# Kernel tuning notes

Hardware: AMD Instinct MI355X
Metric: run time of the kernel (lower is better)

## Reference

```python
import jax, jax.numpy as jnp
import numpy as np
from functools import lru_cache
from jax.scipy.linalg import expm

N_QUBITS = 6
DIM = 2 ** N_QUBITS          # 64
N_PAULI = 4 ** N_QUBITS      # 4096


@lru_cache(maxsize=None)
def _pauli_tensor_np(n_qubits):
    # All n-qubit Pauli strings as dense matrices, ordered base-4
    # (digit 0..3 -> I, X, Y, Z; most-significant digit = first qubit).
    I = np.eye(2, dtype=np.complex64)
    X = np.array([[0, 1], [1, 0]], dtype=np.complex64)
    Y = np.array([[0, -1j], [1j, 0]], dtype=np.complex64)
    Z = np.array([[1, 0], [0, -1]], dtype=np.complex64)
    base = np.stack([I, X, Y, Z])  # [4,2,2]
    T = base
    for _ in range(n_qubits - 1):
        k, d = T.shape[0], T.shape[1]
        T = np.einsum('iab,jcd->ijacbd', T, base).reshape(k * 4, d * 2, d * 2)
    return np.ascontiguousarray(T.astype(np.complex64))  # [4^n, 2^n, 2^n]


def setup_inputs() -> dict:
    key = jax.random.key(0)
    kx, kw, kb = jax.random.split(key, 3)
    x = jax.random.normal(kx, (512, 4000), dtype=jnp.float32)
    weight = jax.random.normal(kw, (4, N_PAULI - 1), dtype=jnp.float32)
    bias = jax.random.normal(kb, (DIM,), dtype=jnp.float32)
    return {"x": x, "weight": weight, "bias": bias}


def reference(x, weight, bias):
    # x: [B, in_dim] float32; weight: [n_reps, 4^n - 1]; bias: [out_dim]
    B, in_dim = x.shape
    n_reps = weight.shape[0]
    out_dim = bias.shape[0]
    P = jnp.asarray(_pauli_tensor_np(N_QUBITS))  # [4096, 64, 64] complex64

    # Pad data coefficients up to the full Pauli basis (identity included).
    xp = jnp.pad(x, ((0, 0), (0, N_PAULI - in_dim))).astype(jnp.complex64)

    # Data-encoding Hamiltonian per sample: H_d[b] = sum_p x[b,p] * P[p]
    Hd = jnp.einsum('bp,pij->bij', xp, P)                       # [B,64,64]
    Ud = jax.vmap(expm)(-1j * Hd)                               # [B,64,64]

    # Trainable Hamiltonians per rep (identity Pauli excluded -> global phase).
    Hp = jnp.einsum('rp,pij->rij', weight.astype(jnp.complex64), P[1:])
    Up = jax.vmap(expm)(-1j * Hp)                               # [R,64,64]

    # Data re-uploading circuit on |0...0>: repeat (U_param @ U_data).
    psi = jnp.zeros((B, DIM), dtype=jnp.complex64).at[:, 0].set(1.0)
    for r in range(n_reps):
        psi = jnp.einsum('bij,bj->bi', Ud, psi)
        psi = jnp.einsum('ij,bj->bi', Up[r], psi)

    # Observables are computational-basis projectors |k><k|, k < out_dim:
    # <psi|O_k|psi> = |psi_k|^2
    probs = (psi[:, :out_dim].real ** 2 + psi[:, :out_dim].imag ** 2)
    return probs.astype(jnp.float32) + bias
```

## Files before the change

kernel.cpp:

```cpp
#include <hip/hip_runtime.h>
#include <math.h>

typedef float2 cplx;
typedef __attribute__((ext_vector_type(8))) short short8v;
typedef __attribute__((ext_vector_type(4))) short short4v;
typedef __attribute__((ext_vector_type(4))) float float4v;

#define IN_DIM 4000
#define NREPS 4

#define C0f  1.0f
#define C1f  1.0f
#define C2f  0.5f
#define C3f  0.16666667f
#define C4f  0.041666668f
#define C5f  8.3333333e-3f
#define C6f  1.3888889e-3f
#define C7f  1.9841270e-4f
#define C8f  2.4801587e-5f
#define C9f  2.7557319e-6f
#define C10f 2.7557319e-7f
#define C11f 2.5052108e-8f
#define C12f 2.0876757e-9f
#define C13f 1.6059044e-10f
#define C14f 1.1470746e-11f
#define C15f 7.6471637e-13f

#define MFMA(A,B,C) __builtin_amdgcn_mfma_f32_16x16x32_bf16((A),(B),(C),0,0,0)


__device__ __forceinline__ int idxSw(int a, int b) {
    return (a << 6) + ((((b >> 3) + a) & 7) << 3) + (b & 7);
}
__device__ __forceinline__ short f2bf(float f) {
    unsigned u = __float_as_uint(f);
    return (short)((u + 0x7FFF + ((u >> 16) & 1)) >> 16);
}
__device__ __forceinline__ float bf2f(short s) {
    return __uint_as_float(((unsigned)(unsigned short)s) << 16);
}
__device__ __forceinline__ short8v neg8(short8v a) {
    int4 u; __builtin_memcpy(&u, &a, 16);
    u.x ^= 0x80008000; u.y ^= 0x80008000; u.z ^= 0x80008000; u.w ^= 0x80008000;
    short8v r; __builtin_memcpy(&r, &u, 16); return r;
}

template<int AM, int BM, int NDM, int NDN>
__device__ __forceinline__ void mm_mfma(const short* __restrict__ As,
                                        const short* __restrict__ Bs,
                                        int li, int q, int mb, int nb,
                                        float4v* __restrict__ accR,
                                        float4v* __restrict__ accI)
{
    #pragma unroll
    for (int ks = 0; ks < 2; ks++) {
        const int ch = ks * 4 + q;
        short8v arh[NDM], arl[NDM], cRh[NDM], cRl[NDM], cIh[NDM], cIl[NDM];
        #pragma unroll
        for (int dm = 0; dm < NDM; dm++) {
            int r = ((mb + dm) << 4) + li;
            int off = (r << 6) + (((ch + r) & 7) << 3);
            arh[dm] = *(const short8v*)(As + off);
            arl[dm] = *(const short8v*)(As + 4096 + off);
            short8v aih = *(const short8v*)(As + 8192 + off);
            short8v ail = *(const short8v*)(As + 12288 + off);
            short8v nih = neg8(aih), nil_ = neg8(ail);
            cRh[dm] = (AM == 2) ? aih : nih;
            cRl[dm] = (AM == 2) ? ail : nil_;
            cIh[dm] = (AM == 2) ? nih : aih;
            cIl[dm] = (AM == 2) ? nil_ : ail;
        }
        #pragma unroll
        for (int dn = 0; dn < NDN; dn++) {
            int n = ((nb + dn) << 4) + li;
            int off = (n << 6) + (((ch + n) & 7) << 3);
            short8v brh = *(const short8v*)(Bs + off);
            short8v brl = *(const short8v*)(Bs + 4096 + off);
            short8v bih = *(const short8v*)(Bs + 8192 + off);
            short8v bil = *(const short8v*)(Bs + 12288 + off);
            if (BM == 1) { brh = neg8(brh); brl = neg8(brl); }
            __builtin_amdgcn_s_setprio(1);
            #pragma unroll
            for (int dm = 0; dm < NDM; dm++) {
                int ti = dm * NDN + dn;
                accR[ti] = MFMA(arh[dm], brh, accR[ti]);
                accR[ti] = MFMA(arh[dm], brl, accR[ti]);
                accR[ti] = MFMA(arl[dm], brh, accR[ti]);
                accR[ti] = MFMA(cRh[dm], bih, accR[ti]);
                accR[ti] = MFMA(cRh[dm], bil, accR[ti]);
                accR[ti] = MFMA(cRl[dm], bih, accR[ti]);
                accI[ti] = MFMA(arh[dm], bih, accI[ti]);
                accI[ti] = MFMA(arh[dm], bil, accI[ti]);
                accI[ti] = MFMA(arl[dm], bih, accI[ti]);
                accI[ti] = MFMA(cIh[dm], brh, accI[ti]);
                accI[ti] = MFMA(cIh[dm], brl, accI[ti]);
                accI[ti] = MFMA(cIl[dm], brh, accI[ti]);
            }
            __builtin_amdgcn_s_setprio(0);
        }
    }
}

template<int NDM, int NDN>
__device__ __forceinline__ void write_row(short* __restrict__ S, int li, int q,
                                          int mb, int nb,
                                          const float4v* cre, const float4v* cim)
{
    #pragma unroll
    for (int dm = 0; dm < NDM; dm++)
    #pragma unroll
    for (int dn = 0; dn < NDN; dn++) {
        int ti = dm * NDN + dn;
        int c = ((nb + dn) << 4) + li;
        #pragma unroll
        for (int reg = 0; reg < 4; reg++) {
            int r = ((mb + dm) << 4) + q * 4 + reg;
            int off = idxSw(r, c);
            float vr = cre[ti][reg], vi = cim[ti][reg];
            short rh = f2bf(vr), rl = f2bf(vr - bf2f(rh));
            short ih = f2bf(vi), il = f2bf(vi - bf2f(ih));
            S[off] = rh; S[4096 + off] = rl; S[8192 + off] = ih; S[12288 + off] = il;
        }
    }
}

template<int NDM, int NDN>
__device__ __forceinline__ void write_rowT(short* __restrict__ S, int li, int q,
                                           int mb, int nb,
                                           const float4v* cre, const float4v* cim)
{
    #pragma unroll
    for (int dm = 0; dm < NDM; dm++)
    #pragma unroll
    for (int dn = 0; dn < NDN; dn++) {
        int ti = dm * NDN + dn;
        int c = ((nb + dn) << 4) + li;
        int k0 = ((mb + dm) << 4) + q * 4;
        int off = idxSw(c, k0);
        short4v rh, rl, ih, il;
        #pragma unroll
        for (int reg = 0; reg < 4; reg++) {
            float vr = cre[ti][reg], vi = cim[ti][reg];
            short h1 = f2bf(vr); rh[reg] = h1; rl[reg] = f2bf(vr - bf2f(h1));
            short h2 = f2bf(vi); ih[reg] = h2; il[reg] = f2bf(vi - bf2f(h2));
        }
        *(short4v*)(S + off) = rh;
        *(short4v*)(S + 4096 + off) = rl;
        *(short4v*)(S + 8192 + off) = ih;
        *(short4v*)(S + 12288 + off) = il;
    }
}

template<int NDM, int NDN>
__device__ __forceinline__ void gather_tile(const short* __restrict__ S, int li, int q,
                                            int mb, int nb, float4v* bre, float4v* bim)
{
    #pragma unroll
    for (int dm = 0; dm < NDM; dm++)
    #pragma unroll
    for (int dn = 0; dn < NDN; dn++) {
        int ti = dm * NDN + dn;
        int c = ((nb + dn) << 4) + li;
        #pragma unroll
        for (int reg = 0; reg < 4; reg++) {
            int r = ((mb + dm) << 4) + q * 4 + reg;
            int off = idxSw(r, c);
            bre[ti][reg] = bf2f(S[off]) + bf2f(S[4096 + off]);
            bim[ti][reg] = bf2f(S[8192 + off]) + bf2f(S[12288 + off]);
        }
    }
}

template<int NDM, int NDN>
__device__ __forceinline__ void adddiag(float4v* u, float cI, int li, int q, int mb, int nb)
{
    #pragma unroll
    for (int dm = 0; dm < NDM; dm++)
    #pragma unroll
    for (int dn = 0; dn < NDN; dn++) {
        if (mb + dm == nb + dn) {
            #pragma unroll
            for (int e = 0; e < 4; e++)
                if (li == q * 4 + e) u[dm * NDN + dn][e] += cI;
        }
    }
}

template<int NDM, int NDN>
__device__ __forceinline__ void store_tiles(cplx* __restrict__ dst, int li, int q,
                                            int mb, int nb,
                                            const float4v* ure, const float4v* uim)
{
    #pragma unroll
    for (int dm = 0; dm < NDM; dm++)
    #pragma unroll
    for (int dn = 0; dn < NDN; dn++) {
        int ti = dm * NDN + dn;
        int c = ((nb + dn) << 4) + li;
        int cs = c ^ (((c >> 4) & 1) << 1);
        #pragma unroll
        for (int reg = 0; reg < 4; reg++) {
            int r = ((mb + dm) << 4) + q * 4 + reg;
            dst[(r << 6) + cs] = make_float2(ure[ti][reg], uim[ti][reg]);
        }
    }
}

__device__ __forceinline__ cplx pauli_phase(float v, int xm, int zm) {
    int ny = __popc(xm & zm) & 3;
    if (ny == 0) return make_float2(v, 0.f);
    if (ny == 1) return make_float2(0.f, -v);
    if (ny == 2) return make_float2(-v, 0.f);
    return make_float2(0.f, v);
}

__device__ __forceinline__ void expm_core8(char* __restrict__ LDS,
                                           const float* __restrict__ src, bool isW,
                                           int t, float4v* ure, float4v* uim)
{
    constexpr int NDM = 1, NDN = 2, NT = 2;
    short* S0 = (short*)LDS;
    short* S1 = (short*)(LDS + 32768);
    cplx*  W  = (cplx*)(LDS + 32768);
    float* red = (float*)(LDS + 65536);
    const int lane = t & 63, wv = t >> 6;
    const int li = lane & 15, q = lane >> 4;
    const int mb = wv & 3, nb = (wv >> 2) << 1;

    float sumsq = 0.f;
    #pragma unroll
    for (int n = 0; n < 8; n++) {
        int p = t + 512 * n;
        int xm = 0, zm = 0;
        #pragma unroll
        for (int k = 0; k < 6; k++) {
            int d = (p >> (2 * k)) & 3;
            int hi = d >> 1, lo = d & 1;
            zm |= hi << k; xm |= (hi ^ lo) << k;
        }
        float v = isW ? ((p == 0) ? 0.f : src[p - 1])
                      : ((p < IN_DIM) ? src[p] : 0.f);
        sumsq += v * v;
        W[(xm << 6) + zm] = pauli_phase(v, xm, zm);
    }
    #pragma unroll
    for (int d = 32; d >= 1; d >>= 1) sumsq += __shfl_xor(sumsq, d, 64);
    if (lane == 0) red[wv] = sumsq;
    __syncthreads();

    float rs = 0.f;
    #pragma unroll
    for (int i2 = 0; i2 < 8; i2++) rs += red[i2];
    float fro = sqrtf(64.f * rs);
    int s1 = 0; { float nn = fro; while (nn > 8.f && s1 < 24) { nn *= 0.5f; s1++; } }
    float sc1 = exp2f((float)(-s1));

    cplx hv[8];
    #pragma unroll
    for (int rr = 0; rr < 8; rr++) hv[rr] = W[((wv * 8 + rr) << 6) + lane];
    #pragma unroll
    for (int d = 1; d < 64; d <<= 1) {
        float sg = (lane & d) ? -1.f : 1.f;
        #pragma unroll
        for (int rr = 0; rr < 8; rr++) {
            float px = __shfl_xor(hv[rr].x, d, 64);
            float py = __shfl_xor(hv[rr].y, d, 64);
            hv[rr].x = fmaf(sg, hv[rr].x, px);
            hv[rr].y = fmaf(sg, hv[rr].y, py);
        }
    }

    #pragma unroll
    for (int rr = 0; rr < 8; rr++) {
        int m = wv * 8 + rr;
        int c = lane ^ m;
        float vr = hv[rr].y * sc1, vi = -hv[rr].x * sc1;
        short rh = f2bf(vr), rl = f2bf(vr - bf2f(rh));
        short ih = f2bf(vi), il = f2bf(vi - bf2f(ih));
        int off = idxSw(lane, c);
        S0[off] = rh; S0[4096 + off] = rl; S0[8192 + off] = ih; S0[12288 + off] = il;
    }
    __syncthreads();

    const float4v z4 = {0.f, 0.f, 0.f, 0.f};
    float4v accR[NT], accI[NT];
    #define ZERO_ACC _Pragma("unroll") for (int i2 = 0; i2 < NT; i2++) { accR[i2]=z4; accI[i2]=z4; }

    ZERO_ACC
    mm_mfma<0, 1, NDM, NDN>(S0, S0, li, q, mb, nb, accR, accI);
    float ss = 0.f;
    #pragma unroll
    for (int ti = 0; ti < NT; ti++)
        #pragma unroll
        for (int e = 0; e < 4; e++)
            ss += accR[ti][e]*accR[ti][e] + accI[ti][e]*accI[ti][e];
    #pragma unroll
    for (int d = 32; d >= 1; d >>= 1) ss += __shfl_xor(ss, d, 64);
    if (lane == 0) red[8 + wv] = ss;
    __syncthreads();

    rs = 0.f;
    #pragma unroll
    for (int i2 = 0; i2 < 8; i2++) rs += red[8 + i2];
    float bound = sqrtf(sqrtf(rs));
    int ds = 0; { float nn = bound; while (nn > 3.4f && ds < 12) { nn *= 0.5f; ds++; } }
    const int s = s1 + ds;
    float dsc = exp2f((float)(-ds)), dsc2 = dsc * dsc;

    float4v bre[NT], bim[NT];
    gather_tile<NDM, NDN>(S0, li, q, mb, nb, bre, bim);

    #pragma unroll
    for (int ti = 0; ti < NT; ti++) { ure[ti] = accR[ti] * dsc2; uim[ti] = accI[ti] * dsc2; }
    write_rowT<NDM, NDN>(S1, li, q, mb, nb, ure, uim);
    __syncthreads();

    {
        float ca = C15f * dsc;
        #pragma unroll
        for (int ti = 0; ti < NT; ti++) { ure[ti] = ca * bre[ti]; uim[ti] = ca * bim[ti]; }
        adddiag<NDM, NDN>(ure, C14f, li, q, mb, nb);
        write_rowT<NDM, NDN>(S0, li, q, mb, nb, ure, uim);
    }
    __syncthreads();

    const float cIc[7] = { C0f, C2f, C4f, C6f, C8f, C10f, C12f };
    const float cAc[7] = { C1f, C3f, C5f, C7f, C9f, C11f, C13f };
    for (int j = 6; j >= 0; j--) {
        ZERO_ACC
        mm_mfma<2, 0, NDM, NDN>(S1, S0, li, q, mb, nb, accR, accI);
        __syncthreads();
        float ca = cAc[j] * dsc, cI = cIc[j];
        #pragma unroll
        for (int ti = 0; ti < NT; ti++) {
            ure[ti] = accR[ti] + ca * bre[ti];
            uim[ti] = accI[ti] + ca * bim[ti];
        }
        adddiag<NDM, NDN>(ure, cI, li, q, mb, nb);
        write_rowT<NDM, NDN>(S0, li, q, mb, nb, ure, uim);
        __syncthreads();
    }

    for (int sq = 0; sq < s; sq++) {
        write_row<NDM, NDN>(S1, li, q, mb, nb, ure, uim);
        if (sq > 0) write_rowT<NDM, NDN>(S0, li, q, mb, nb, ure, uim);
        __syncthreads();
        ZERO_ACC
        mm_mfma<0, 0, NDM, NDN>(S1, S0, li, q, mb, nb, accR, accI);
        __syncthreads();
        #pragma unroll
        for (int ti = 0; ti < NT; ti++) { ure[ti] = accR[ti]; uim[ti] = accI[ti]; }
    }
    #undef ZERO_ACC
}

__device__ __forceinline__ cplx matvec_wave8(const cplx* __restrict__ M,
                                             const cplx* __restrict__ pin,
                                             int lane, int wv)
{
    const int ri = lane & 7;
    const int rr = (wv << 3) + ri;
    const int kc = lane >> 3;
    const int ch = (kc + ri) & 7;
    const int b  = (ch >> 1) & 1;
    const float4* Mr = (const float4*)(M + (rr << 6)) + (ch << 2);
    float4 m0 = Mr[0 ^ b], m1 = Mr[1 ^ b], m2 = Mr[2 ^ b], m3 = Mr[3 ^ b];
    const cplx* p = pin + (ch << 3);
    cplx p0 = p[0], p1 = p[1], p2 = p[2], p3 = p[3];
    cplx p4 = p[4], p5 = p[5], p6 = p[6], p7 = p[7];
    float ax = 0.f, ay = 0.f;
    ax = fmaf(m0.x, p0.x, fmaf(-m0.y, p0.y, ax));
    ay = fmaf(m0.x, p0.y, fmaf( m0.y, p0.x, ay));
    ax = fmaf(m0.z, p1.x, fmaf(-m0.w, p1.y, ax));
    ay = fmaf(m0.z, p1.y, fmaf( m0.w, p1.x, ay));
    ax = fmaf(m1.x, p2.x, fmaf(-m1.y, p2.y, ax));
    ay = fmaf(m1.x, p2.y, fmaf( m1.y, p2.x, ay));
    ax = fmaf(m1.z, p3.x, fmaf(-m1.w, p3.y, ax));
    ay = fmaf(m1.z, p3.y, fmaf( m1.w, p3.x, ay));
    ax = fmaf(m2.x, p4.x, fmaf(-m2.y, p4.y, ax));
    ay = fmaf(m2.x, p4.y, fmaf( m2.y, p4.x, ay));
    ax = fmaf(m2.z, p5.x, fmaf(-m2.w, p5.y, ax));
    ay = fmaf(m2.z, p5.y, fmaf( m2.w, p5.x, ay));
    ax = fmaf(m3.x, p6.x, fmaf(-m3.y, p6.y, ax));
    ay = fmaf(m3.x, p6.y, fmaf( m3.y, p6.x, ay));
    ax = fmaf(m3.z, p7.x, fmaf(-m3.w, p7.y, ax));
    ay = fmaf(m3.z, p7.y, fmaf( m3.w, p7.x, ay));
    ax += __shfl_xor(ax, 8, 64);  ay += __shfl_xor(ay, 8, 64);
    ax += __shfl_xor(ax, 16, 64); ay += __shfl_xor(ay, 16, 64);
    ax += __shfl_xor(ax, 32, 64); ay += __shfl_xor(ay, 32, 64);
    return make_float2(ax, ay);
}

__global__ __launch_bounds__(512, 4) void circuit_kernel(const float* __restrict__ x,
                                                         const float* __restrict__ w,
                                                         const float* __restrict__ bias,
                                                         cplx* __restrict__ ws,
                                                         int* __restrict__ flag,
                                                         float* __restrict__ out)
{
    __shared__ float4 LDSf4[4168];
    char* LDS = (char*)LDSf4;
    const int t = threadIdx.x, b = blockIdx.x;
    const int lane = t & 63, wv = t >> 6, li = lane & 15, q = lane >> 4;
    const int mb = wv & 3, nb = (wv >> 2) << 1;
    float4v ure[2], uim[2];

    for (int duty = (b < NREPS) ? 0 : 1; duty < 2; duty++) {
        const bool isW = (duty == 0);
        const float* src = isW ? (w + (size_t)b * 4095) : (x + (size_t)b * IN_DIM);
        expm_core8(LDS, src, isW, t, ure, uim);
        if (isW) {
            store_tiles<1, 2>(ws + ((size_t)b << 12), li, q, mb, nb, ure, uim);
            __syncthreads();
            if (t == 0)
                __hip_atomic_fetch_add(flag, 1, __ATOMIC_RELEASE, __HIP_MEMORY_SCOPE_AGENT);
        }
    }

    cplx* Ud   = (cplx*)(LDS + 32768);
    cplx* UpS  = (cplx*)LDS;
    cplx* psiA = (cplx*)(LDS + 65664);
    cplx* psiB = (cplx*)(LDS + 66176);

    store_tiles<1, 2>(Ud, li, q, mb, nb, ure, uim);
    if (t < 64) psiA[t] = make_float2(t == 0 ? 1.f : 0.f, 0.f);
    if (t == 0) {
        while (__hip_atomic_load(flag, __ATOMIC_ACQUIRE, __HIP_MEMORY_SCOPE_AGENT) < NREPS)
            __builtin_amdgcn_s_sleep(8);
    }
    __syncthreads();

    const int rowi = (wv << 3) + (lane & 7);
    for (int r = 0; r < NREPS; r++) {
        {
            const float4* srcv = (const float4*)(ws + ((size_t)r << 12));
            float4* dstY = (float4*)UpS;
            #pragma unroll
            for (int n = 0; n < 4; n++) dstY[n * 512 + t] = srcv[n * 512 + t];
        }
        cplx v1 = matvec_wave8(Ud, psiA, lane, wv);
        if (lane < 8) psiB[rowi] = v1;
        __syncthreads();
        cplx v2 = matvec_wave8(UpS, psiB, lane, wv);
        if (lane < 8) psiA[rowi] = v2;
        __syncthreads();
    }
    if (t < 64) {
        cplx pv = psiA[t];
        out[(b << 6) + t] = fmaf(pv.x, pv.x, fmaf(pv.y, pv.y, bias[t]));
    }
}

extern "C" void kernel_launch(void* const* d_in, const int* in_sizes, int n_in,
                              void* d_out, int out_size, void* d_ws, size_t ws_size,
                              hipStream_t stream)
{
    const float* x    = (const float*)d_in[0];
    const float* w    = (const float*)d_in[1];
    const float* bias = (const float*)d_in[2];
    float* out = (float*)d_out;
    cplx* ws   = (cplx*)d_ws;
    int* flag  = (int*)((char*)d_ws + (NREPS << 15));

    int B = in_sizes[0] / IN_DIM;

    hipMemsetAsync(flag, 0, sizeof(int), stream);
    hipLaunchKernelGGL(circuit_kernel, dim3(B), dim3(512), 0, stream,
                       x, w, bias, ws, flag, out);
}
```

Measured before the change: 153.8 us.

## Split parameter-unitary expm into separate 1024-thread kernel, drop in-kernel flag spin

Moves the four trainable-Hamiltonian matrix exponentials out of the fused circuit kernel into a separate up_kernel with 1024 threads (16 waves, one 16x16 tile each) and 128KB LDS. The main kernel no longer has blocks 0-3 doing double work or blocks spinning on an atomic flag, and the memset is removed. The cost is an extra kernel launch and a serialization point between the kernels: the data expm can no longer overlap with the parameter expm.

```diff
diff --git a/kernel.cpp b/kernel.cpp
--- a/kernel.cpp
+++ b/kernel.cpp
@@ -44,6 +44,15 @@
     u.x ^= 0x80008000; u.y ^= 0x80008000; u.z ^= 0x80008000; u.w ^= 0x80008000;
     short8v r; __builtin_memcpy(&r, &u, 16); return r;
 }
+
+__device__ __forceinline__ cplx pauli_phase(float v, int xm, int zm) {
+    int ny = __popc(xm & zm) & 3;
+    if (ny == 0) return make_float2(v, 0.f);
+    if (ny == 1) return make_float2(0.f, -v);
+    if (ny == 2) return make_float2(-v, 0.f);
+    return make_float2(0.f, v);
+}
+
 
 template<int AM, int BM, int NDM, int NDN>
 __device__ __forceinline__ void mm_mfma(const short* __restrict__ As,
@@ -206,14 +215,6 @@
     }
 }
 
-__device__ __forceinline__ cplx pauli_phase(float v, int xm, int zm) {
-    int ny = __popc(xm & zm) & 3;
-    if (ny == 0) return make_float2(v, 0.f);
-    if (ny == 1) return make_float2(0.f, -v);
-    if (ny == 2) return make_float2(-v, 0.f);
-    return make_float2(0.f, v);
-}
-
 __device__ __forceinline__ void expm_core8(char* __restrict__ LDS,
                                            const float* __restrict__ src, bool isW,
                                            int t, float4v* ure, float4v* uim)
@@ -269,7 +270,6 @@
             hv[rr].y = fmaf(sg, hv[rr].y, py);
         }
     }
-
     #pragma unroll
     for (int rr = 0; rr < 8; rr++) {
         int m = wv * 8 + rr;
@@ -350,6 +350,257 @@
         __syncthreads();
         #pragma unroll
         for (int ti = 0; ti < NT; ti++) { ure[ti] = accR[ti]; uim[ti] = accI[ti]; }
+    }
+    #undef ZERO_ACC
+}
+
+
+template<int AM, int BM>
+__device__ __forceinline__ void mm_mfma1(const short* __restrict__ As,
+                                         const short* __restrict__ Bs,
+                                         int li, int q, int mb, int nb,
+                                         float4v* __restrict__ accR,
+                                         float4v* __restrict__ accI)
+{
+    #pragma unroll
+    for (int ks = 0; ks < 2; ks++) {
+        const int ch = ks * 4 + q;
+        int r = (mb << 4) + li;
+        int offA = (r << 6) + (((ch + r) & 7) << 3);
+        short8v arh = *(const short8v*)(As + offA);
+        short8v arl = *(const short8v*)(As + 4096 + offA);
+        short8v aih = *(const short8v*)(As + 8192 + offA);
+        short8v ail = *(const short8v*)(As + 12288 + offA);
+        short8v nih = neg8(aih), nil_ = neg8(ail);
+        short8v cRh = (AM == 2) ? aih : nih;
+        short8v cRl = (AM == 2) ? ail : nil_;
+        short8v cIh = (AM == 2) ? nih : aih;
+        short8v cIl = (AM == 2) ? nil_ : ail;
+
+        int n = (nb << 4) + li;
+        int offB = (n << 6) + (((ch + n) & 7) << 3);
+        short8v brh = *(const short8v*)(Bs + offB);
+        short8v brl = *(const short8v*)(Bs + 4096 + offB);
+        short8v bih = *(const short8v*)(Bs + 8192 + offB);
+        short8v bil = *(const short8v*)(Bs + 12288 + offB);
+        if (BM == 1) { brh = neg8(brh); brl = neg8(brl); }
+
+        accR[0] = MFMA(arh, brh, accR[0]);
+        accR[0] = MFMA(arh, brl, accR[0]);
+        accR[0] = MFMA(arl, brh, accR[0]);
+        accR[0] = MFMA(cRh, bih, accR[0]);
+        accR[0] = MFMA(cRh, bil, accR[0]);
+        accR[0] = MFMA(cRl, bih, accR[0]);
+        accI[0] = MFMA(arh, bih, accI[0]);
+        accI[0] = MFMA(arh, bil, accI[0]);
+        accI[0] = MFMA(arl, bih, accI[0]);
+        accI[0] = MFMA(cIh, brh, accI[0]);
+        accI[0] = MFMA(cIh, brl, accI[0]);
+        accI[0] = MFMA(cIl, brh, accI[0]);
+    }
+}
+
+__device__ __forceinline__ void write_row1(short* __restrict__ S, int li, int q,
+                                           int mb, int nb,
+                                           const float4v* cre, const float4v* cim)
+{
+    int c = (nb << 4) + li;
+    #pragma unroll
+    for (int reg = 0; reg < 4; reg++) {
+        int r = (mb << 4) + q * 4 + reg;
+        int off = idxSw(r, c);
+        float vr = cre[0][reg], vi = cim[0][reg];
+        short rh = f2bf(vr), rl = f2bf(vr - bf2f(rh));
+        short ih = f2bf(vi), il = f2bf(vi - bf2f(ih));
+        S[off] = rh; S[4096 + off] = rl; S[8192 + off] = ih; S[12288 + off] = il;
+    }
+}
+
+__device__ __forceinline__ void write_rowT1(short* __restrict__ S, int li, int q,
+                                            int mb, int nb,
+                                            const float4v* cre, const float4v* cim)
+{
+    int c = (nb << 4) + li;
+    int k0 = (mb << 4) + q * 4;
+    int off = idxSw(c, k0);
+    short4v rh, rl, ih, il;
+    #pragma unroll
+    for (int reg = 0; reg < 4; reg++) {
+        float vr = cre[0][reg], vi = cim[0][reg];
+        short h1 = f2bf(vr); rh[reg] = h1; rl[reg] = f2bf(vr - bf2f(h1));
+        short h2 = f2bf(vi); ih[reg] = h2; il[reg] = f2bf(vi - bf2f(h2));
+    }
+    *(short4v*)(S + off) = rh;
+    *(short4v*)(S + 4096 + off) = rl;
+    *(short4v*)(S + 8192 + off) = ih;
+    *(short4v*)(S + 12288 + off) = il;
+}
+
+__device__ __forceinline__ void gather_tile1(const short* __restrict__ S, int li, int q,
+                                             int mb, int nb, float4v* bre, float4v* bim)
+{
+    int c = (nb << 4) + li;
+    #pragma unroll
+    for (int reg = 0; reg < 4; reg++) {
+        int r = (mb << 4) + q * 4 + reg;
+        int off = idxSw(r, c);
+        bre[0][reg] = bf2f(S[off]) + bf2f(S[4096 + off]);
+        bim[0][reg] = bf2f(S[8192 + off]) + bf2f(S[12288 + off]);
+    }
+}
+
+__device__ __forceinline__ void adddiag1(float4v* u, float cI, int li, int q, int mb, int nb)
+{
+    if (mb == nb) {
+        #pragma unroll
+        for (int e = 0; e < 4; e++)
+            if (li == q * 4 + e) u[0][e] += cI;
+    }
+}
+
+__device__ __forceinline__ void store_tiles1(cplx* __restrict__ dst, int li, int q,
+                                             int mb, int nb,
+                                             const float4v* ure, const float4v* uim)
+{
+    int c = (nb << 4) + li;
+    int cs = c ^ (((c >> 4) & 1) << 1);
+    #pragma unroll
+    for (int reg = 0; reg < 4; reg++) {
+        int r = (mb << 4) + q * 4 + reg;
+        dst[(r << 6) + cs] = make_float2(ure[0][reg], uim[0][reg]);
+    }
+}
+
+__device__ __forceinline__ void expm_core16(char* __restrict__ LDS,
+                                            const float* __restrict__ src, bool isW,
+                                            int t, float4v* ure, float4v* uim)
+{
+    short* P0 = (short*)LDS;
+    short* P1 = (short*)(LDS + 32768);
+    short* P2 = (short*)(LDS + 65536);
+    short* P3 = (short*)(LDS + 98304);
+    cplx*  W  = (cplx*)(LDS + 65536);
+    float* red = (float*)(LDS + 98304);
+    const int lane = t & 63, wv = t >> 6;
+    const int li = lane & 15, q = lane >> 4;
+    const int mb = wv & 3, nb = wv >> 2;
+
+    float sumsq = 0.f;
+    #pragma unroll
+    for (int n = 0; n < 4; n++) {
+        int p = t + 1024 * n;
+        int xm = 0, zm = 0;
+        #pragma unroll
+        for (int k = 0; k < 6; k++) {
+            int d = (p >> (2 * k)) & 3;
+            int hi = d >> 1, lo = d & 1;
+            zm |= hi << k; xm |= (hi ^ lo) << k;
+        }
+        float v = isW ? ((p == 0) ? 0.f : src[p - 1])
+                      : ((p < IN_DIM) ? src[p] : 0.f);
+        sumsq += v * v;
+        W[(xm << 6) + zm] = pauli_phase(v, xm, zm);
+    }
+    #pragma unroll
+    for (int d = 32; d >= 1; d >>= 1) sumsq += __shfl_xor(sumsq, d, 64);
+    if (lane == 0) red[wv] = sumsq;
+    __syncthreads();
+
+    float rs = 0.f;
+    #pragma unroll
+    for (int i2 = 0; i2 < 16; i2++) rs += red[i2];
+    float fro = sqrtf(64.f * rs);
+    int s1 = 0; { float nn = fro; while (nn > 8.f && s1 < 24) { nn *= 0.5f; s1++; } }
+    float sc1 = exp2f((float)(-s1));
+
+    cplx hv[4];
+    #pragma unroll
+    for (int rr = 0; rr < 4; rr++) hv[rr] = W[((wv * 4 + rr) << 6) + lane];
+    #pragma unroll
+    for (int d = 1; d < 64; d <<= 1) {
+        float sg = (lane & d) ? -1.f : 1.f;
+        #pragma unroll
+        for (int rr = 0; rr < 4; rr++) {
+            float px = __shfl_xor(hv[rr].x, d, 64);
+            float py = __shfl_xor(hv[rr].y, d, 64);
+            hv[rr].x = fmaf(sg, hv[rr].x, px);
+            hv[rr].y = fmaf(sg, hv[rr].y, py);
+        }
+    }
+    #pragma unroll
+    for (int rr = 0; rr < 4; rr++) {
+        int m = wv * 4 + rr;
+        int c = lane ^ m;
+        float vr = hv[rr].y * sc1, vi = -hv[rr].x * sc1;
+        short rh = f2bf(vr), rl = f2bf(vr - bf2f(rh));
+        short ih = f2bf(vi), il = f2bf(vi - bf2f(ih));
+        int off = idxSw(lane, c);
+        P0[off] = rh; P0[4096 + off] = rl; P0[8192 + off] = ih; P0[12288 + off] = il;
+    }
+    __syncthreads();
+
+    const float4v z4 = {0.f, 0.f, 0.f, 0.f};
+    float4v accR[1], accI[1];
+    #define ZERO_ACC { accR[0] = z4; accI[0] = z4; }
+
+    ZERO_ACC
+    mm_mfma1<0, 1>(P0, P0, li, q, mb, nb, accR, accI);
+    write_rowT1(P1, li, q, mb, nb, accR, accI);
+    float ss = 0.f;
+    #pragma unroll
+    for (int e = 0; e < 4; e++)
+        ss += accR[0][e]*accR[0][e] + accI[0][e]*accI[0][e];
+    #pragma unroll
+    for (int d = 32; d >= 1; d >>= 1) ss += __shfl_xor(ss, d, 64);
+    if (lane == 0) red[16 + wv] = ss;
+    __syncthreads();
+
+    rs = 0.f;
+    #pragma unroll
+    for (int i2 = 0; i2 < 16; i2++) rs += red[16 + i2];
+    float bound = sqrtf(sqrtf(rs));
+    int ds = 0; { float nn = bound; while (nn > 3.4f && ds < 12) { nn *= 0.5f; ds++; } }
+    const int s = s1 + ds;
+    float dsc = exp2f((float)(-ds)), dsc2 = dsc * dsc;
+
+    float4v bre[1], bim[1];
+    gather_tile1(P0, li, q, mb, nb, bre, bim);
+
+    {
+        float ca = C15f * dsc;
+        ure[0] = ca * bre[0]; uim[0] = ca * bim[0];
+        adddiag1(ure, C14f, li, q, mb, nb);
+        write_rowT1(P2, li, q, mb, nb, ure, uim);
+    }
+    __syncthreads();
+
+    const float cIc[7] = { C0f, C2f, C4f, C6f, C8f, C10f, C12f };
+    const float cAc[7] = { C1f, C3f, C5f, C7f, C9f, C11f, C13f };
+    short* Vr = P2; short* Vw = P3;
+    for (int j = 6; j >= 0; j--) {
+        ZERO_ACC
+        mm_mfma1<2, 0>(P1, Vr, li, q, mb, nb, accR, accI);
+        float ca = cAc[j] * dsc, cI = cIc[j];
+        ure[0] = dsc2 * accR[0] + ca * bre[0];
+        uim[0] = dsc2 * accI[0] + ca * bim[0];
+        adddiag1(ure, cI, li, q, mb, nb);
+        if (j > 0) {
+            write_rowT1(Vw, li, q, mb, nb, ure, uim);
+            short* tmp = Vr; Vr = Vw; Vw = tmp;
+        }
+        __syncthreads();
+    }
+
+    for (int sq = 0; sq < s; sq++) {
+        short* Ua = (sq & 1) ? P2 : P0;
+        short* Ub = (sq & 1) ? P3 : P1;
+        write_row1(Ua, li, q, mb, nb, ure, uim);
+        write_rowT1(Ub, li, q, mb, nb, ure, uim);
+        __syncthreads();
+        ZERO_ACC
+        mm_mfma1<0, 0>(Ua, Ub, li, q, mb, nb, accR, accI);
+        __syncthreads();
+        ure[0] = accR[0]; uim[0] = accI[0];
     }
     #undef ZERO_ACC
 }
@@ -391,11 +642,22 @@
     return make_float2(ax, ay);
 }
 
+__global__ __launch_bounds__(1024) void up_kernel(const float* __restrict__ w,
+                                                  cplx* __restrict__ ws)
+{
+    __shared__ float4 LDSf4[8192];
+    char* LDS = (char*)LDSf4;
+    const int t = threadIdx.x, r = blockIdx.x;
+    const int lane = t & 63, wv = t >> 6, li = lane & 15, q = lane >> 4;
+    const int mb = wv & 3, nb = wv >> 2;
+    float4v ure[1], uim[1];
+    expm_core16(LDS, w + (size_t)r * 4095, true, t, ure, uim);
+    store_tiles1(ws + ((size_t)r << 12), li, q, mb, nb, ure, uim);
+}
+
 __global__ __launch_bounds__(512, 4) void circuit_kernel(const float* __restrict__ x,
-                                                         const float* __restrict__ w,
+                                                         const cplx* __restrict__ ws,
                                                          const float* __restrict__ bias,
-                                                         cplx* __restrict__ ws,
-                                                         int* __restrict__ flag,
                                                          float* __restrict__ out)
 {
     __shared__ float4 LDSf4[4168];
@@ -405,17 +667,7 @@
     const int mb = wv & 3, nb = (wv >> 2) << 1;
     float4v ure[2], uim[2];
 
-    for (int duty = (b < NREPS) ? 0 : 1; duty < 2; duty++) {
-        const bool isW = (duty == 0);
-        const float* src = isW ? (w + (size_t)b * 4095) : (x + (size_t)b * IN_DIM);
-        expm_core8(LDS, src, isW, t, ure, uim);
-        if (isW) {
-            store_tiles<1, 2>(ws + ((size_t)b << 12), li, q, mb, nb, ure, uim);
-            __syncthreads();
-            if (t == 0)
-                __hip_atomic_fetch_add(flag, 1, __ATOMIC_RELEASE, __HIP_MEMORY_SCOPE_AGENT);
-        }
-    }
+    expm_core8(LDS, x + (size_t)b * IN_DIM, false, t, ure, uim);
 
     cplx* Ud   = (cplx*)(LDS + 32768);
     cplx* UpS  = (cplx*)LDS;
@@ -424,10 +676,6 @@
 
     store_tiles<1, 2>(Ud, li, q, mb, nb, ure, uim);
     if (t < 64) psiA[t] = make_float2(t == 0 ? 1.f : 0.f, 0.f);
-    if (t == 0) {
-        while (__hip_atomic_load(flag, __ATOMIC_ACQUIRE, __HIP_MEMORY_SCOPE_AGENT) < NREPS)
-            __builtin_amdgcn_s_sleep(8);
-    }
     __syncthreads();
 
     const int rowi = (wv << 3) + (lane & 7);
@@ -460,11 +708,9 @@
     const float* bias = (const float*)d_in[2];
     float* out = (float*)d_out;
     cplx* ws   = (cplx*)d_ws;
-    int* flag  = (int*)((char*)d_ws + (NREPS << 15));
 
     int B = in_sizes[0] / IN_DIM;
 
-    hipMemsetAsync(flag, 0, sizeof(int), stream);
-    hipLaunchKernelGGL(circuit_kernel, dim3(B), dim3(512), 0, stream,
-                       x, w, bias, ws, flag, out);
-}
+    hipLaunchKernelGGL(up_kernel,      dim3(NREPS), dim3(1024), 0, stream, w, ws);
+    hipLaunchKernelGGL(circuit_kernel, dim3(B),     dim3(512),  0, stream, x, ws, bias, out);
+}
```

Result: faster. 146.7 us (-4.6%).
